# Kernel optimization log

Measured on AMD Instinct MI355X. Metric: run time of the kernel, lower is better.

The kernel has to match this reference:

```python
import jax, jax.numpy as jnp
import numpy as np

T, H, N, Q, C = 65536, 768, 32768, 32768, 10
MAX_LEN = 16  # max span length


def _make_spans(key, n):
    k1, k2 = jax.random.split(key)
    starts = jax.random.randint(k1, (n,), 0, T - MAX_LEN)
    lengths = jax.random.randint(k2, (n,), 1, MAX_LEN + 1)
    return jnp.stack([starts, starts + lengths], axis=1)  # [start, end)


def setup_inputs() -> dict:
    key = jax.random.key(0)
    ks = jax.random.split(key, 6)
    token_emb = jax.random.normal(ks[0], (T, H), dtype=jnp.float32)
    spans_support = _make_spans(ks[1], N)
    labels = jax.random.randint(ks[2], (N,), 0, C)
    spans_query = _make_spans(ks[3], Q)
    W_proj = jax.random.normal(ks[4], (3 * H, H), dtype=jnp.float32) * (1.0 / np.sqrt(3 * H))
    b_proj = jnp.zeros((H,), dtype=jnp.float32)
    return dict(token_emb=token_emb, spans_support=spans_support, labels=labels,
                spans_query=spans_query, W_proj=W_proj, b_proj=b_proj, n_classes=C)


def _span_embed(token_emb, spans, W, b):
    # token_emb: (T, H); spans: (n, 2) [start, end)
    s = spans[:, 0]
    e = spans[:, 1]
    # exclusive-prefix-sum trick turns per-span mean pooling into two gathers
    zero = jnp.zeros((1, token_emb.shape[1]), token_emb.dtype)
    csum = jnp.concatenate([zero, jnp.cumsum(token_emb, axis=0)], axis=0)  # (T+1, H)
    h_mean = (csum[e] - csum[s]) / (e - s).astype(token_emb.dtype)[:, None]
    feat = jnp.concatenate([token_emb[s], token_emb[e - 1], h_mean], axis=-1)  # (n, 3H)
    return jax.nn.gelu(feat @ W + b, approximate=False)  # torch nn.GELU default = erf


def _l2norm(x, eps=1e-12):
    # matches torch F.normalize: x / max(||x||, eps)
    return x / jnp.maximum(jnp.linalg.norm(x, axis=-1, keepdims=True), eps)


def reference(token_emb, spans_support, labels, spans_query, W_proj, b_proj, n_classes):
    sup = _span_embed(token_emb, spans_support, W_proj, b_proj)  # (N, H)
    qry = _span_embed(token_emb, spans_query, W_proj, b_proj)    # (Q, H)
    # prototypes = per-class mean; empty classes fall back to global mean
    sums = jax.ops.segment_sum(sup, labels, num_segments=n_classes)           # (C, H)
    counts = jax.ops.segment_sum(jnp.ones((sup.shape[0],), sup.dtype), labels,
                                 num_segments=n_classes)                       # (C,)
    gmean = sup.mean(axis=0)
    protos = jnp.where(counts[:, None] > 0,
                       sums / jnp.maximum(counts, 1.0)[:, None],
                       gmean[None, :])
    # cosine metric + constant NONE logit of 0.5
    sim = _l2norm(qry) @ _l2norm(protos).T                                     # (Q, C)
    none_logit = jnp.full((qry.shape[0], 1), 0.5, dtype=qry.dtype)
    return jnp.concatenate([sim, none_logit], axis=-1)                         # (Q, C+1)
```

## Files before the change

### kernel.cpp

```cpp
#include <hip/hip_runtime.h>
#include <stdint.h>

#define H_DIM 768
#define N_SUP 32768
#define Q_QRY 32768
#define C_CLS 10
#define M_TOT 65536
#define KG 768
#define NG 2304
#define NT 12
#define NBUCK 1024

typedef __bf16 bf16x8 __attribute__((ext_vector_type(8)));
typedef float f32x4 __attribute__((ext_vector_type(4)));
typedef __attribute__((address_space(3))) void lds_void;
typedef const __attribute__((address_space(1))) void g_void;

__device__ __forceinline__ ushort f2bf(float f) {
  union { float f; uint32_t u; } v; v.f = f;
  uint32_t r = (v.u + 0x7FFFu + ((v.u >> 16) & 1u)) >> 16;
  return (ushort)r;
}
__device__ __forceinline__ float bf2f(ushort h) {
  union { uint32_t u; float f; } v; v.u = ((uint32_t)h) << 16; return v.f;
}
__device__ __forceinline__ float gelu_f(float x) {
  return 0.5f * x * (1.0f + erff(x * 0.70710678118654752f));
}

__global__ void prep_kernel(const float* __restrict__ te, const float* __restrict__ W,
                            const int* __restrict__ spS, const int* __restrict__ spQ,
                            ushort* __restrict__ tb, ushort* __restrict__ Bt,
                            int* __restrict__ hist) {
  int b = blockIdx.x, t = threadIdx.x;
  if (b < 24576) {
    size_t i = (((size_t)b * 256) + t) * 8;
    float4 v0 = *(const float4*)(te + i);
    float4 v1 = *(const float4*)(te + i + 4);
    ushort4 o0, o1;
    o0.x = f2bf(v0.x); o0.y = f2bf(v0.y); o0.z = f2bf(v0.z); o0.w = f2bf(v0.w);
    o1.x = f2bf(v1.x); o1.y = f2bf(v1.y); o1.z = f2bf(v1.z); o1.w = f2bf(v1.w);
    *(ushort4*)(tb + i) = o0;
    *(ushort4*)(tb + i + 4) = o1;
  } else if (b < 31488) {
    int idx = (b - 24576) * 256 + t;
    int n = idx / KG, k = idx - n * KG;
    int blk = n / H_DIM;
    int c = n - blk * H_DIM;
    Bt[idx] = f2bf(W[(size_t)(blk * H_DIM + k) * H_DIM + c]);
  } else {
    __shared__ int lh[NBUCK];
    for (int i = t; i < NBUCK; i += 256) lh[i] = 0;
    __syncthreads();
    int b0 = b - 31488;
    for (int i = b0 * 256 + t; i < M_TOT; i += 64 * 256) {
      int s = (i < N_SUP) ? spS[2 * i] : spQ[2 * (i - N_SUP)];
      atomicAdd(&lh[s >> 6], 1);
    }
    __syncthreads();
    for (int i = t; i < NBUCK; i += 256) if (lh[i]) atomicAdd(&hist[i], lh[i]);
  }
}

__global__ void prefix_kernel(const int* __restrict__ hist, int* __restrict__ cursor) {
  __shared__ int tmp[NBUCK];
  int t = threadIdx.x;
  int v = hist[t];
  tmp[t] = v;
  __syncthreads();
  for (int off = 1; off < NBUCK; off <<= 1) {
    int add = (t >= off) ? tmp[t - off] : 0;
    __syncthreads();
    tmp[t] += add;
    __syncthreads();
  }
  cursor[t] = tmp[t] - v;
}

__global__ void scatter_kernel(const int* __restrict__ spS, const int* __restrict__ spQ,
                               int* __restrict__ cursor, int2* __restrict__ sorted) {
  for (int i = blockIdx.x * 256 + threadIdx.x; i < M_TOT; i += gridDim.x * 256) {
    int s, e;
    if (i < N_SUP) { s = spS[2 * i]; e = spS[2 * i + 1]; }
    else           { int w = i - N_SUP; s = spQ[2 * w]; e = spQ[2 * w + 1]; }
    int pos = atomicAdd(&cursor[s >> 6], 1);
    int2 rec; rec.x = s; rec.y = (i << 5) | (e - s);
    sorted[pos] = rec;
  }
}

__global__ __launch_bounds__(512, 2) void gemm8(const ushort* __restrict__ A,
                                                const ushort* __restrict__ Bt,
                                                ushort* __restrict__ C) {
  __shared__ ushort lds[65536];
  char* ldsc = (char*)lds;

  int orig = blockIdx.x;
  int wg = (orig & 7) * 288 + (orig >> 3);
  int rowT = wg / 9, colT = wg - rowT * 9;
  int m0 = rowT * 256, n0 = colT * 256;

  int tid = threadIdx.x;
  int lane = tid & 63, wave = tid >> 6;
  int wr = wave >> 2, wc = wave & 3;
  int l15 = lane & 15, l4 = lane >> 4;

  int row0 = tid >> 2;
  int ss = (tid & 3) ^ ((row0 >> 1) & 3);
  size_t eA0 = (size_t)(m0 + row0) * KG + ss * 8;
  size_t eA1 = (size_t)(m0 + row0 + 128) * KG + ss * 8;
  size_t eB0 = (size_t)(n0 + row0) * KG + ss * 8;
  size_t eB1 = (size_t)(n0 + row0 + 128) * KG + ss * 8;

  int aoff[8], boff[4];
#pragma unroll
  for (int m = 0; m < 8; ++m) {
    int r = wr * 128 + m * 16 + l15;
    aoff[m] = r * 64 + ((l4 ^ ((r >> 1) & 3)) << 4);
  }
#pragma unroll
  for (int n = 0; n < 4; ++n) {
    int r = wc * 64 + n * 16 + l15;
    boff[n] = r * 64 + ((l4 ^ ((r >> 1) & 3)) << 4);
  }

  f32x4 acc[8][4];
#pragma unroll
  for (int m = 0; m < 8; ++m)
#pragma unroll
    for (int n = 0; n < 4; ++n) acc[m][n] = (f32x4){0.f, 0.f, 0.f, 0.f};

#define SLOT_A(kh, db) (ldsc + ((kh) * 2 + (db)) * 16384)
#define SLOT_B(kh, db) (ldsc + 65536 + ((kh) * 2 + (db)) * 16384)
#define STAGE_A(tk, kh, db) do { \
    char* _d = SLOT_A(kh, db) + wave * 1024; \
    size_t _k = (size_t)(tk) * 64 + (kh) * 32; \
    __builtin_amdgcn_global_load_lds((g_void*)(A + eA0 + _k), (lds_void*)_d, 16, 0, 0); \
    __builtin_amdgcn_global_load_lds((g_void*)(A + eA1 + _k), (lds_void*)(_d + 8192), 16, 0, 0); \
  } while (0)
#define STAGE_B(tk, kh, db) do { \
    char* _d = SLOT_B(kh, db) + wave * 1024; \
    size_t _k = (size_t)(tk) * 64 + (kh) * 32; \
    __builtin_amdgcn_global_load_lds((g_void*)(Bt + eB0 + _k), (lds_void*)_d, 16, 0, 0); \
    __builtin_amdgcn_global_load_lds((g_void*)(Bt + eB1 + _k), (lds_void*)(_d + 8192), 16, 0, 0); \
  } while (0)
#define LDA4(base, o) do { _Pragma("unroll") for (int m = 0; m < 4; ++m) \
    af[m] = *reinterpret_cast<const bf16x8*>((base) + aoff[(o) + m]); } while (0)
#define LDB4(base) do { _Pragma("unroll") for (int n = 0; n < 4; ++n) \
    bf[n] = *reinterpret_cast<const bf16x8*>((base) + boff[n]); } while (0)
#define MFMA_BLOCK(MB) do { _Pragma("unroll") for (int m = 0; m < 4; ++m) \
  _Pragma("unroll") for (int n = 0; n < 4; ++n) \
    acc[(MB) + m][n] = __builtin_amdgcn_mfma_f32_16x16x32_bf16(af[m], bf[n], acc[(MB) + m][n], 0, 0, 0); \
  } while (0)
#define BARX() __builtin_amdgcn_s_barrier()
#define LGKM0() asm volatile("s_waitcnt lgkmcnt(0)" ::: "memory")
#define VM8() asm volatile("s_waitcnt vmcnt(8)" ::: "memory")

  STAGE_A(0, 0, 0); STAGE_B(0, 0, 0);
  STAGE_A(0, 1, 0); STAGE_B(0, 1, 0);
  STAGE_A(1, 0, 1); STAGE_B(1, 0, 1);
  VM8();
  BARX();

  bf16x8 af[4], bf[4];
  for (int t = 0; t < NT; ++t) {
    int d = t & 1, nd = d ^ 1;
    int tk1 = (t + 1 < NT) ? t + 1 : NT - 1;
    int tk2 = (t + 2 < NT) ? t + 2 : NT - 1;
    const char* Ak0 = SLOT_A(0, d); const char* Bk0 = SLOT_B(0, d);
    const char* Ak1 = SLOT_A(1, d); const char* Bk1 = SLOT_B(1, d);
    LDA4(Ak0, 0); LDB4(Bk0);
    STAGE_A(tk1, 1, nd);
    BARX(); LGKM0();
    __builtin_amdgcn_s_setprio(1); MFMA_BLOCK(0); __builtin_amdgcn_s_setprio(0);
    BARX();
    LDA4(Ak0, 4);
    STAGE_B(tk1, 1, nd);
    BARX(); LGKM0();
    __builtin_amdgcn_s_setprio(1); MFMA_BLOCK(4); __builtin_amdgcn_s_setprio(0);
    VM8(); BARX();
    LDA4(Ak1, 0); LDB4(Bk1);
    STAGE_A(tk2, 0, d);
    BARX(); LGKM0();
    __builtin_amdgcn_s_setprio(1); MFMA_BLOCK(0); __builtin_amdgcn_s_setprio(0);
    BARX();
    LDA4(Ak1, 4);
    STAGE_B(tk2, 0, d);
    BARX(); LGKM0();
    __builtin_amdgcn_s_setprio(1); MFMA_BLOCK(4); __builtin_amdgcn_s_setprio(0);
    VM8(); BARX();
  }
  asm volatile("s_waitcnt vmcnt(0)" ::: "memory");

#pragma unroll
  for (int m = 0; m < 8; ++m)
#pragma unroll
    for (int n = 0; n < 4; ++n) {
      int col = n0 + wc * 64 + n * 16 + l15;
      size_t rb = (size_t)(m0 + wr * 128 + m * 16 + l4 * 4) * NG + col;
#pragma unroll
      for (int v = 0; v < 4; ++v)
        C[rb + (size_t)v * NG] = f2bf(acc[m][n][v]);
    }
#undef SLOT_A
#undef SLOT_B
#undef STAGE_A
#undef STAGE_B
#undef LDA4
#undef LDB4
#undef MFMA_BLOCK
}

__global__ __launch_bounds__(256) void combine2(const ushort* __restrict__ PQR,
                                                const int2* __restrict__ sorted,
                                                const float* __restrict__ bias,
                                                ushort* __restrict__ emb) {
  int b = blockIdx.x;
  int sb = ((b & 7) << 11) + (b >> 3);
  int wave = threadIdx.x >> 6, lane = threadIdx.x & 63;
  int wid = sb * 4 + wave;
  int2 rec = sorted[wid];
  int s = rec.x;
  int len = rec.y & 31;
  int orig = rec.y >> 5;
  int e = s + len;
  float inv = 1.0f / (float)len;

  float acc0[3][4], accr[3][4];
  const ushort* Pr = PQR + (size_t)s * NG;
  const ushort* Qr = PQR + (size_t)(e - 1) * NG + 768;
#pragma unroll
  for (int c = 0; c < 3; ++c) {
    int h = c * 256 + lane * 4;
    ushort4 p = *(const ushort4*)(Pr + h);
    ushort4 q = *(const ushort4*)(Qr + h);
    acc0[c][0] = bf2f(p.x) + bf2f(q.x);
    acc0[c][1] = bf2f(p.y) + bf2f(q.y);
    acc0[c][2] = bf2f(p.z) + bf2f(q.z);
    acc0[c][3] = bf2f(p.w) + bf2f(q.w);
    accr[c][0] = accr[c][1] = accr[c][2] = accr[c][3] = 0.f;
  }
  for (int r = s; r < e; ++r) {
    const ushort* Rr = PQR + (size_t)r * NG + 1536;
#pragma unroll
    for (int c = 0; c < 3; ++c) {
      int h = c * 256 + lane * 4;
      ushort4 rv = *(const ushort4*)(Rr + h);
      accr[c][0] += bf2f(rv.x); accr[c][1] += bf2f(rv.y);
      accr[c][2] += bf2f(rv.z); accr[c][3] += bf2f(rv.w);
    }
  }
  ushort* er = emb + (size_t)orig * H_DIM;
#pragma unroll
  for (int c = 0; c < 3; ++c) {
    int h = c * 256 + lane * 4;
    float4 bv = *(const float4*)(bias + h);
    ushort4 o;
    o.x = f2bf(gelu_f(acc0[c][0] + accr[c][0] * inv + bv.x));
    o.y = f2bf(gelu_f(acc0[c][1] + accr[c][1] * inv + bv.y));
    o.z = f2bf(gelu_f(acc0[c][2] + accr[c][2] * inv + bv.z));
    o.w = f2bf(gelu_f(acc0[c][3] + accr[c][3] * inv + bv.w));
    *(ushort4*)(er + h) = o;
  }
}

__global__ void proto_accum(const ushort* __restrict__ supEmb, const int* __restrict__ labels,
                            float* __restrict__ pSum, float* __restrict__ pCnt) {
  __shared__ float ls[C_CLS * H_DIM];
  __shared__ int lc[C_CLS];
  int t = threadIdx.x;
  for (int i = t; i < C_CLS * H_DIM; i += 256) ls[i] = 0.f;
  if (t < C_CLS) lc[t] = 0;
  __syncthreads();
  int base = blockIdx.x * 128;
  for (int si = 0; si < 128; ++si) {
    int sp = base + si;
    int lab = labels[sp];
    const ushort* er = supEmb + (size_t)sp * H_DIM;
#pragma unroll
    for (int j = 0; j < 3; ++j) {
      int c = t + j * 256;
      ls[lab * H_DIM + c] += bf2f(er[c]);
    }
    if (t == 0) lc[lab]++;
  }
  __syncthreads();
  for (int i = t; i < C_CLS * H_DIM; i += 256) atomicAdd(&pSum[i], ls[i]);
  if (t < C_CLS) atomicAdd(&pCnt[t], (float)lc[t]);
}

__global__ void proto_norm(const float* __restrict__ pSum, const float* __restrict__ pCnt,
                           float* __restrict__ pN) {
  __shared__ float red[4];
  int t = threadIdx.x, lane = t & 63, wave = t >> 6;
  for (int c = 0; c < C_CLS; ++c) {
    float cnt = pCnt[c];
    float x[3];
#pragma unroll
    for (int j = 0; j < 3; ++j) {
      int h = t + j * 256;
      float v;
      if (cnt > 0.5f) v = pSum[c * H_DIM + h] / cnt;
      else {
        float gs = 0.f;
        for (int cc = 0; cc < C_CLS; ++cc) gs += pSum[cc * H_DIM + h];
        v = gs / (float)N_SUP;
      }
      x[j] = v;
    }
    float ss = x[0] * x[0] + x[1] * x[1] + x[2] * x[2];
#pragma unroll
    for (int o = 32; o; o >>= 1) ss += __shfl_xor(ss, o);
    if (lane == 0) red[wave] = ss;
    __syncthreads();
    float tot = red[0] + red[1] + red[2] + red[3];
    float inv = 1.0f / fmaxf(sqrtf(tot), 1e-12f);
#pragma unroll
    for (int j = 0; j < 3; ++j) pN[c * H_DIM + t + j * 256] = x[j] * inv;
    __syncthreads();
  }
}

__global__ void sim_kernel(const ushort* __restrict__ emb, const float* __restrict__ pN,
                           float* __restrict__ out) {
  __shared__ float lp[C_CLS * H_DIM];
  int t = threadIdx.x;
  for (int i = t; i < C_CLS * H_DIM; i += 256) lp[i] = pN[i];
  __syncthreads();
  int lane = t & 63, wave = t >> 6;
  for (int row = blockIdx.x * 4 + wave; row < Q_QRY; row += gridDim.x * 4) {
    const ushort* qr = emb + (size_t)(N_SUP + row) * H_DIM;
    float dot[C_CLS] = {0, 0, 0, 0, 0, 0, 0, 0, 0, 0};
    float sq = 0.f;
#pragma unroll
    for (int j = 0; j < 12; ++j) {
      float v = bf2f(qr[lane + 64 * j]);
      sq += v * v;
#pragma unroll
      for (int p = 0; p < C_CLS; ++p) dot[p] += v * lp[p * H_DIM + lane + 64 * j];
    }
#pragma unroll
    for (int o = 32; o; o >>= 1) {
      sq += __shfl_xor(sq, o);
#pragma unroll
      for (int p = 0; p < C_CLS; ++p) dot[p] += __shfl_xor(dot[p], o);
    }
    if (lane == 0) {
      float inv = 1.0f / fmaxf(sqrtf(sq), 1e-12f);
      float* o = out + (size_t)row * (C_CLS + 1);
      o[0] = dot[0] * inv; o[1] = dot[1] * inv; o[2] = dot[2] * inv;
      o[3] = dot[3] * inv; o[4] = dot[4] * inv; o[5] = dot[5] * inv;
      o[6] = dot[6] * inv; o[7] = dot[7] * inv; o[8] = dot[8] * inv;
      o[9] = dot[9] * inv; o[10] = 0.5f;
    }
  }
}

extern "C" void kernel_launch(void* const* d_in, const int* in_sizes, int n_in,
                              void* d_out, int out_size, void* d_ws, size_t ws_size,
                              hipStream_t stream) {
  const float* token_emb = (const float*)d_in[0];
  const int*   spansS    = (const int*)d_in[1];
  const int*   labels    = (const int*)d_in[2];
  const int*   spansQ    = (const int*)d_in[3];
  const float* W         = (const float*)d_in[4];
  const float* b         = (const float*)d_in[5];
  float* out = (float*)d_out;

  char* ws = (char*)d_ws;
  size_t pqrB = (size_t)M_TOT * NG * 2;
  size_t embB = (size_t)M_TOT * H_DIM * 2;
  size_t wtB  = (size_t)NG * KG * 2;
  ushort* PQR  = (ushort*)ws;
  ushort* tebf = (ushort*)(ws + pqrB);
  ushort* emb  = tebf;
  ushort* Bt   = (ushort*)(ws + pqrB + embB);
  char*   tail = ws + pqrB + embB + wtB;
  float*  pSum = (float*)tail;
  float*  pCnt = pSum + C_CLS * H_DIM;
  float*  pN   = pCnt + 64;
  int*    hist = (int*)(pN + C_CLS * H_DIM);
  int*    cursor = hist + NBUCK;
  int2*   sorted = (int2*)(cursor + NBUCK);

  hipMemsetAsync(pSum, 0, (C_CLS * H_DIM + 64) * sizeof(float), stream);
  hipMemsetAsync(hist, 0, NBUCK * sizeof(int), stream);
  prep_kernel<<<31552, 256, 0, stream>>>(token_emb, W, spansS, spansQ, tebf, Bt, hist);
  prefix_kernel<<<1, NBUCK, 0, stream>>>(hist, cursor);
  scatter_kernel<<<64, 256, 0, stream>>>(spansS, spansQ, cursor, sorted);
  gemm8<<<2304, 512, 0, stream>>>(tebf, Bt, PQR);
  combine2<<<16384, 256, 0, stream>>>(PQR, sorted, b, emb);
  proto_accum<<<N_SUP / 128, 256, 0, stream>>>(emb, labels, pSum, pCnt);
  proto_norm<<<1, 256, 0, stream>>>(pSum, pCnt, pN);
  sim_kernel<<<512, 256, 0, stream>>>(emb, pN, out);
}
```

Baseline: 598.9 us.

## Gather span features before the GEMM and fuse bias+GELU into its epilogue

The order of the work is reversed. A new kernel first builds the per-span feature matrix (start token, end token, mean over the span) of width 2304 from the bf16 token embeddings. A single GEMM with K=2304 and N=768 then applies the bias and erf-GELU directly in its epilogue. This removes the wide per-token projection buffer of width 2304 and the separate combine pass that gathered from it, with the same FLOP count. The costs are a large gathered feature buffer that must be written and then re-read, and a GEMM grid of only 768 tiles, which can leave part of the last wave idle.

```diff
diff --git a/kernel.cpp b/kernel.cpp
--- a/kernel.cpp
+++ b/kernel.cpp
@@ -6,9 +6,9 @@
 #define Q_QRY 32768
 #define C_CLS 10
 #define M_TOT 65536
-#define KG 768
-#define NG 2304
-#define NT 12
+#define KGB 2304
+#define NGB 768
+#define NT 36
 #define NBUCK 1024
 
 typedef __bf16 bf16x8 __attribute__((ext_vector_type(8)));
@@ -44,10 +44,8 @@
     *(ushort4*)(tb + i + 4) = o1;
   } else if (b < 31488) {
     int idx = (b - 24576) * 256 + t;
-    int n = idx / KG, k = idx - n * KG;
-    int blk = n / H_DIM;
-    int c = n - blk * H_DIM;
-    Bt[idx] = f2bf(W[(size_t)(blk * H_DIM + k) * H_DIM + c]);
+    int n = idx / KGB, k = idx - n * KGB;
+    Bt[idx] = f2bf(W[(size_t)k * H_DIM + n]);
   } else {
     __shared__ int lh[NBUCK];
     for (int i = t; i < NBUCK; i += 256) lh[i] = 0;
@@ -89,15 +87,62 @@
   }
 }
 
+__global__ __launch_bounds__(256) void feat_build(const ushort* __restrict__ te,
+                                                  const int2* __restrict__ sorted,
+                                                  ushort* __restrict__ feat) {
+  int b = blockIdx.x;
+  int sb = ((b & 7) << 11) + (b >> 3);
+  int wave = threadIdx.x >> 6, lane = threadIdx.x & 63;
+  int wid = sb * 4 + wave;
+  int2 rec = sorted[wid];
+  int s = rec.x, len = rec.y & 31, orig = rec.y >> 5;
+  int e = s + len;
+  float inv = 1.0f / (float)len;
+
+  ushort4 first[3], last[3];
+  float accr[3][4];
+  const ushort* Fr = te + (size_t)s * H_DIM;
+  const ushort* Lr = te + (size_t)(e - 1) * H_DIM;
+#pragma unroll
+  for (int c = 0; c < 3; ++c) {
+    int h = c * 256 + lane * 4;
+    first[c] = *(const ushort4*)(Fr + h);
+    last[c]  = *(const ushort4*)(Lr + h);
+    accr[c][0] = accr[c][1] = accr[c][2] = accr[c][3] = 0.f;
+  }
+  for (int r = s; r < e; ++r) {
+    const ushort* Rr = te + (size_t)r * H_DIM;
+#pragma unroll
+    for (int c = 0; c < 3; ++c) {
+      int h = c * 256 + lane * 4;
+      ushort4 rv = *(const ushort4*)(Rr + h);
+      accr[c][0] += bf2f(rv.x); accr[c][1] += bf2f(rv.y);
+      accr[c][2] += bf2f(rv.z); accr[c][3] += bf2f(rv.w);
+    }
+  }
+  ushort* fr = feat + (size_t)orig * KGB;
+#pragma unroll
+  for (int c = 0; c < 3; ++c) {
+    int h = c * 256 + lane * 4;
+    ushort4 m;
+    m.x = f2bf(accr[c][0] * inv); m.y = f2bf(accr[c][1] * inv);
+    m.z = f2bf(accr[c][2] * inv); m.w = f2bf(accr[c][3] * inv);
+    *(ushort4*)(fr + h) = first[c];
+    *(ushort4*)(fr + 768 + h) = last[c];
+    *(ushort4*)(fr + 1536 + h) = m;
+  }
+}
+
 __global__ __launch_bounds__(512, 2) void gemm8(const ushort* __restrict__ A,
                                                 const ushort* __restrict__ Bt,
-                                                ushort* __restrict__ C) {
+                                                const float* __restrict__ bias,
+                                                ushort* __restrict__ emb) {
   __shared__ ushort lds[65536];
   char* ldsc = (char*)lds;
 
   int orig = blockIdx.x;
-  int wg = (orig & 7) * 288 + (orig >> 3);
-  int rowT = wg / 9, colT = wg - rowT * 9;
+  int wg = (orig & 7) * 96 + (orig >> 3);
+  int rowT = wg / 3, colT = wg - rowT * 3;
   int m0 = rowT * 256, n0 = colT * 256;
 
   int tid = threadIdx.x;
@@ -107,10 +152,10 @@
 
   int row0 = tid >> 2;
   int ss = (tid & 3) ^ ((row0 >> 1) & 3);
-  size_t eA0 = (size_t)(m0 + row0) * KG + ss * 8;
-  size_t eA1 = (size_t)(m0 + row0 + 128) * KG + ss * 8;
-  size_t eB0 = (size_t)(n0 + row0) * KG + ss * 8;
-  size_t eB1 = (size_t)(n0 + row0 + 128) * KG + ss * 8;
+  size_t eA0 = (size_t)(m0 + row0) * KGB + ss * 8;
+  size_t eA1 = (size_t)(m0 + row0 + 128) * KGB + ss * 8;
+  size_t eB0 = (size_t)(n0 + row0) * KGB + ss * 8;
+  size_t eB1 = (size_t)(n0 + row0 + 128) * KGB + ss * 8;
 
   int aoff[8], boff[4];
 #pragma unroll
@@ -197,10 +242,13 @@
 #pragma unroll
     for (int n = 0; n < 4; ++n) {
       int col = n0 + wc * 64 + n * 16 + l15;
-      size_t rb = (size_t)(m0 + wr * 128 + m * 16 + l4 * 4) * NG + col;
-#pragma unroll
-      for (int v = 0; v < 4; ++v)
-        C[rb + (size_t)v * NG] = f2bf(acc[m][n][v]);
+      float bc = bias[col];
+      size_t rb = (size_t)(m0 + wr * 128 + m * 16 + l4 * 4) * NGB + col;
+#pragma unroll
+      for (int v = 0; v < 4; ++v) {
+        float x = acc[m][n][v] + bc;
+        emb[rb + (size_t)v * NGB] = f2bf(gelu_f(x));
+      }
     }
 #undef SLOT_A
 #undef SLOT_B
@@ -209,59 +257,6 @@
 #undef LDA4
 #undef LDB4
 #undef MFMA_BLOCK
-}
-
-__global__ __launch_bounds__(256) void combine2(const ushort* __restrict__ PQR,
-                                                const int2* __restrict__ sorted,
-                                                const float* __restrict__ bias,
-                                                ushort* __restrict__ emb) {
-  int b = blockIdx.x;
-  int sb = ((b & 7) << 11) + (b >> 3);
-  int wave = threadIdx.x >> 6, lane = threadIdx.x & 63;
-  int wid = sb * 4 + wave;
-  int2 rec = sorted[wid];
-  int s = rec.x;
-  int len = rec.y & 31;
-  int orig = rec.y >> 5;
-  int e = s + len;
-  float inv = 1.0f / (float)len;
-
-  float acc0[3][4], accr[3][4];
-  const ushort* Pr = PQR + (size_t)s * NG;
-  const ushort* Qr = PQR + (size_t)(e - 1) * NG + 768;
-#pragma unroll
-  for (int c = 0; c < 3; ++c) {
-    int h = c * 256 + lane * 4;
-    ushort4 p = *(const ushort4*)(Pr + h);
-    ushort4 q = *(const ushort4*)(Qr + h);
-    acc0[c][0] = bf2f(p.x) + bf2f(q.x);
-    acc0[c][1] = bf2f(p.y) + bf2f(q.y);
-    acc0[c][2] = bf2f(p.z) + bf2f(q.z);
-    acc0[c][3] = bf2f(p.w) + bf2f(q.w);
-    accr[c][0] = accr[c][1] = accr[c][2] = accr[c][3] = 0.f;
-  }
-  for (int r = s; r < e; ++r) {
-    const ushort* Rr = PQR + (size_t)r * NG + 1536;
-#pragma unroll
-    for (int c = 0; c < 3; ++c) {
-      int h = c * 256 + lane * 4;
-      ushort4 rv = *(const ushort4*)(Rr + h);
-      accr[c][0] += bf2f(rv.x); accr[c][1] += bf2f(rv.y);
-      accr[c][2] += bf2f(rv.z); accr[c][3] += bf2f(rv.w);
-    }
-  }
-  ushort* er = emb + (size_t)orig * H_DIM;
-#pragma unroll
-  for (int c = 0; c < 3; ++c) {
-    int h = c * 256 + lane * 4;
-    float4 bv = *(const float4*)(bias + h);
-    ushort4 o;
-    o.x = f2bf(gelu_f(acc0[c][0] + accr[c][0] * inv + bv.x));
-    o.y = f2bf(gelu_f(acc0[c][1] + accr[c][1] * inv + bv.y));
-    o.z = f2bf(gelu_f(acc0[c][2] + accr[c][2] * inv + bv.z));
-    o.w = f2bf(gelu_f(acc0[c][3] + accr[c][3] * inv + bv.w));
-    *(ushort4*)(er + h) = o;
-  }
 }
 
 __global__ void proto_accum(const ushort* __restrict__ supEmb, const int* __restrict__ labels,
@@ -368,14 +363,14 @@
   float* out = (float*)d_out;
 
   char* ws = (char*)d_ws;
-  size_t pqrB = (size_t)M_TOT * NG * 2;
-  size_t embB = (size_t)M_TOT * H_DIM * 2;
-  size_t wtB  = (size_t)NG * KG * 2;
-  ushort* PQR  = (ushort*)ws;
-  ushort* tebf = (ushort*)(ws + pqrB);
+  size_t featB = (size_t)M_TOT * KGB * 2;
+  size_t tbB   = (size_t)M_TOT * H_DIM * 2;
+  size_t wtB   = (size_t)NGB * KGB * 2;
+  ushort* feat = (ushort*)ws;
+  ushort* tebf = (ushort*)(ws + featB);
   ushort* emb  = tebf;
-  ushort* Bt   = (ushort*)(ws + pqrB + embB);
-  char*   tail = ws + pqrB + embB + wtB;
+  ushort* Bt   = (ushort*)(ws + featB + tbB);
+  char*   tail = ws + featB + tbB + wtB;
   float*  pSum = (float*)tail;
   float*  pCnt = pSum + C_CLS * H_DIM;
   float*  pN   = pCnt + 64;
@@ -388,8 +383,8 @@
   prep_kernel<<<31552, 256, 0, stream>>>(token_emb, W, spansS, spansQ, tebf, Bt, hist);
   prefix_kernel<<<1, NBUCK, 0, stream>>>(hist, cursor);
   scatter_kernel<<<64, 256, 0, stream>>>(spansS, spansQ, cursor, sorted);
-  gemm8<<<2304, 512, 0, stream>>>(tebf, Bt, PQR);
-  combine2<<<16384, 256, 0, stream>>>(PQR, sorted, b, emb);
+  feat_build<<<16384, 256, 0, stream>>>(tebf, sorted, feat);
+  gemm8<<<768, 512, 0, stream>>>(feat, Bt, b, emb);
   proto_accum<<<N_SUP / 128, 256, 0, stream>>>(emb, labels, pSum, pCnt);
   proto_norm<<<1, 256, 0, stream>>>(pSum, pCnt, pN);
   sim_kernel<<<512, 256, 0, stream>>>(emb, pN, out);
```

After: 643.8 us. +7.5%, slower.
